# Performance work log

Measured on AMD Instinct MI355X. Metric: run time of the kernel, lower is better.

## Reference

```python
import jax, jax.numpy as jnp
import numpy as np

DEPTH = 6
N_LEAF = 2 ** DEPTH          # 64
GATE_COUNT = N_LEAF - 1      # 63
B = 1024
GATING_FEATURES = 512
IN_FEATURES = 512
OUT_FEATURES = 512


def setup_inputs() -> dict:
    key = jax.random.key(0)
    k1, k2, k3, k4 = jax.random.split(key, 4)
    x_gating = jax.random.normal(k1, (B, GATING_FEATURES), dtype=jnp.float32)
    x_leaf = jax.random.normal(k2, (B, IN_FEATURES), dtype=jnp.float32)
    # kaiming-normal-ish init scales
    gw = jax.random.normal(k3, (GATING_FEATURES, GATE_COUNT), dtype=jnp.float32) * (1.0 / np.sqrt(GATING_FEATURES))
    gb = jnp.zeros((GATE_COUNT,), dtype=jnp.float32)
    pw = jax.random.normal(k4, (OUT_FEATURES, IN_FEATURES, N_LEAF), dtype=jnp.float32) * (1.0 / np.sqrt(IN_FEATURES))
    pb = jnp.zeros((OUT_FEATURES, N_LEAF), dtype=jnp.float32)
    return {"x_gating": x_gating, "x_leaf": x_leaf, "gw": gw, "gb": gb, "pw": pw, "pb": pb}


def _leaf_probs(x_gating, gw, gb):
    # gatings: (B, gate_count), internal nodes in breadth-first order
    gatings = jax.nn.sigmoid(x_gating @ gw + gb)
    b = gatings.shape[0]
    dens = jnp.ones((b, 1), dtype=gatings.dtype)  # root density
    start = 0
    for d in range(DEPTH):
        n_par = 2 ** d
        g = gatings[:, start:start + n_par]          # (B, n_par)
        # left child (even it+1) gets g, right child gets 1-g, interleaved
        dens = jnp.stack([dens * g, dens * (1.0 - g)], axis=-1).reshape(b, 2 * n_par)
        start += n_par
    return dens  # (B, n_leaf) = leaf densities (last n_leaf node densities)


def reference(x_gating, x_leaf, gw, gb, pw, pb):
    leaf_probs = _leaf_probs(x_gating, gw, gb)              # (B, L)
    # gated projection applied to x_leaf, summed over leaves:
    # equals ((pw @ leaf_probs.T).permute(2,0,1) @ x_leaf[...,None])[...,0]
    result = jnp.einsum('oil,bl,bi->bo', pw, leaf_probs, x_leaf)
    result = result + leaf_probs @ pb.T                     # gated bias (B, O)
    return result
```

## Files before the change

### kernel.cpp

```cpp
#include <hip/hip_runtime.h>
#include <stdint.h>

#define B_SZ   1024
#define GF     512
#define GC     63
#define NLEAF  64
#define IN_F   512
#define OUT_F  512

typedef float f32x4 __attribute__((ext_vector_type(4)));
typedef __fp16 h16x2 __attribute__((ext_vector_type(2)));
typedef __fp16 h16x8 __attribute__((ext_vector_type(8)));
typedef _Float16 f16x2 __attribute__((ext_vector_type(2)));

union HF8 { f16x2 h2[4]; h16x8 v; uint4 u; };

__device__ inline f16x2 pkrtz(float a, float b) {
  union { h16x2 r; f16x2 f; } u;
  u.r = __builtin_amdgcn_cvt_pkrtz(a, b);
  return u.f;
}

__global__ __launch_bounds__(512, 2) void k_leafprobs(
    const float* __restrict__ xg, const float* __restrict__ gw,
    const float* __restrict__ gb, float* __restrict__ p_ws)
{
  __shared__ float xsr[GF];
  __shared__ float part[512];
  __shared__ float gates[GC + 1];
  const int b = blockIdx.x;
  const int t = threadIdx.x;

  xsr[t] = xg[(size_t)b * GF + t];
  __syncthreads();

  const int ks = t >> 6, g = t & 63;
  float acc = 0.f;
  if (g < GC) {
    const float* gp = gw + (size_t)(ks * 64) * GC + g;
    const float* xp = &xsr[ks * 64];
#pragma unroll 8
    for (int k = 0; k < 64; ++k) acc += xp[k] * gp[(size_t)k * GC];
  }
  part[t] = acc;
  __syncthreads();

  if (t < GC) {
    float s = gb[t];
#pragma unroll
    for (int r = 0; r < 8; ++r) s += part[r * 64 + t];
    gates[t] = 1.f / (1.f + expf(-s));
  }
  __syncthreads();

  if (t < NLEAF) {
    float v = 1.f;
    int idx = 0, start = 0;
#pragma unroll
    for (int d = 0; d < 6; ++d) {
      int bit = (t >> (5 - d)) & 1;
      float gg = gates[start + idx];
      v *= bit ? (1.f - gg) : gg;
      idx = 2 * idx + bit;
      start += (1 << d);
    }
    p_ws[(size_t)b * NLEAF + t] = v;
  }
}

#define SK 16
#define KI 32

template <bool ATOMIC>
__global__ __launch_bounds__(256, 2) void k_fused(
    const float* __restrict__ x_leaf,
    const float* __restrict__ p_ws,
    const float* __restrict__ pw,
    const float* __restrict__ pb,
    float* __restrict__ dst)
{
  __shared__ __align__(16) float         xs[KI][256];
  __shared__ __align__(16) unsigned char bs8[2 * 16384];

  const int tid  = threadIdx.x;
  const int lane = tid & 63;
  const int wid  = tid >> 6;
  const int quad = lane >> 4;
  const int l15  = lane & 15;
  const int l7   = l15 & 7;

  const int bid = blockIdx.x;
  const int nt  = bid & 7;
  const int mt  = (bid >> 3) & 3;
  const int kc  = bid >> 5;

  const int row_m0 = mt * 256;
  const int o0     = nt * 64;
  const int i0     = kc * KI;
  const int wm     = wid * 64;

  {
    const float* src = x_leaf + (size_t)(row_m0 + tid) * IN_F + i0;
#pragma unroll
    for (int q = 0; q < 8; ++q) {
      float4 v = *(const float4*)(src + q * 4);
      xs[q * 4 + 0][tid] = v.x;
      xs[q * 4 + 1][tid] = v.y;
      xs[q * 4 + 2][tid] = v.z;
      xs[q * 4 + 3][tid] = v.w;
    }
  }

  HF8 prh[4][2];
#pragma unroll
  for (int mi = 0; mi < 4; ++mi) {
    const int row = row_m0 + wm + mi * 16 + l15;
#pragma unroll
    for (int ks = 0; ks < 2; ++ks) {
      const f32x4* src = (const f32x4*)(p_ws + (size_t)row * NLEAF + ks * 32 + quad * 8);
      f32x4 lo = src[0], hi = src[1];
      prh[mi][ks].h2[0] = pkrtz(lo[0], lo[1]);
      prh[mi][ks].h2[1] = pkrtz(lo[2], lo[3]);
      prh[mi][ks].h2[2] = pkrtz(hi[0], hi[1]);
      prh[mi][ks].h2[3] = pkrtz(hi[2], hi[3]);
    }
  }

  const int br  = tid >> 2;
  const int seg = tid & 3;
  const float* bsrc0 = pw + ((size_t)(o0 + br) * IN_F + i0) * NLEAF + seg * 16;

  const int wsw   = (br & 7) << 4;
  const int woff0 = br * 128 + ((seg * 32) ^ wsw);
  const int woff1 = br * 128 + ((seg * 32 + 16) ^ wsw);
  int coff[2];
#pragma unroll
  for (int ks = 0; ks < 2; ++ks)
    coff[ks] = (ks * 64 + quad * 16) ^ (l7 << 4);
  const int rbase = l15 * 128;

  f32x4 acc[4][4];
#pragma unroll
  for (int mi = 0; mi < 4; ++mi)
#pragma unroll
    for (int ni = 0; ni < 4; ++ni)
      acc[mi][ni] = (f32x4)(0.f);

  f32x4 rb[4][4];
  HF8 afA[2][4], afB[2][4];

#define BLOAD(T, SLOT)                                                        \
  {                                                                           \
    const float* a_ = bsrc0 + (size_t)(T) * NLEAF;                            \
    asm volatile(                                                             \
        "global_load_dwordx4 %0, %4, off\n\t"                                 \
        "global_load_dwordx4 %1, %4, off offset:16\n\t"                       \
        "global_load_dwordx4 %2, %4, off offset:32\n\t"                       \
        "global_load_dwordx4 %3, %4, off offset:48"                           \
        : "=&v"(rb[SLOT][0]), "=&v"(rb[SLOT][1]),                             \
          "=&v"(rb[SLOT][2]), "=&v"(rb[SLOT][3])                              \
        : "v"(a_) : "memory");                                                \
  }

#define BWAIT_(SLOT, N)                                                       \
  asm volatile("s_waitcnt vmcnt(" #N ")"                                      \
               : "+v"(rb[SLOT][0]), "+v"(rb[SLOT][1]),                        \
                 "+v"(rb[SLOT][2]), "+v"(rb[SLOT][3])::"memory");
#define BWAIT(SLOT, N) BWAIT_(SLOT, N)

#define BSTAGE(SLOT, BUF, SUB)                                                \
  {                                                                           \
    HF8 c0_, c1_;                                                             \
    f32x4 a0_ = rb[SLOT][0], a1_ = rb[SLOT][1];                               \
    f32x4 a2_ = rb[SLOT][2], a3_ = rb[SLOT][3];                               \
    c0_.h2[0] = pkrtz(a0_[0], a0_[1]);                                        \
    c0_.h2[1] = pkrtz(a0_[2], a0_[3]);                                        \
    c0_.h2[2] = pkrtz(a1_[0], a1_[1]);                                        \
    c0_.h2[3] = pkrtz(a1_[2], a1_[3]);                                        \
    c1_.h2[0] = pkrtz(a2_[0], a2_[1]);                                        \
    c1_.h2[1] = pkrtz(a2_[2], a2_[3]);                                        \
    c1_.h2[2] = pkrtz(a3_[0], a3_[1]);                                        \
    c1_.h2[3] = pkrtz(a3_[2], a3_[3]);                                        \
    unsigned char* d_ = bs8 + (BUF) * 16384 + (SUB) * 8192;                   \
    *(uint4*)(d_ + woff0) = c0_.u;                                            \
    *(uint4*)(d_ + woff1) = c1_.u;                                            \
  }

#define BARRIER() asm volatile("s_waitcnt lgkmcnt(0)\n\ts_barrier" ::: "memory")

#define PREP(IT, AF)                                                          \
  {                                                                           \
    float xvf[4];                                                             \
    _Float16 xh[4];                                                           \
    _Pragma("unroll")                                                         \
    for (int mi = 0; mi < 4; ++mi) xvf[mi] = xs[(IT)][wm + mi * 16 + l15];    \
    _Pragma("unroll")                                                         \
    for (int mi = 0; mi < 4; ++mi) xh[mi] = (_Float16)xvf[mi];                \
    _Pragma("unroll")                                                         \
    for (int ks = 0; ks < 2; ++ks) {                                          \
      _Pragma("unroll")                                                       \
      for (int mi = 0; mi < 4; ++mi) {                                        \
        f16x2 xp_; xp_[0] = xh[mi]; xp_[1] = xh[mi];                          \
        _Pragma("unroll")                                                     \
        for (int j = 0; j < 4; ++j) AF[ks][mi].h2[j] = prh[mi][ks].h2[j] * xp_; \
      }                                                                       \
    }                                                                         \
  }

#define MFMAC(AF, BUF, SUB)                                                   \
  {                                                                           \
    const unsigned char* bsr_ = bs8 + (BUF) * 16384 + (SUB) * 8192;           \
    __builtin_amdgcn_s_setprio(1);                                            \
    _Pragma("unroll")                                                         \
    for (int ks = 0; ks < 2; ++ks) {                                          \
      _Pragma("unroll")                                                       \
      for (int ni = 0; ni < 4; ++ni) {                                        \
        h16x8 bfr = *(const h16x8*)(bsr_ + ni * 2048 + rbase + coff[ks]);     \
        _Pragma("unroll")                                                     \
        for (int mi = 0; mi < 4; ++mi)                                        \
          acc[mi][ni] = __builtin_amdgcn_mfma_f32_16x16x32_f16(               \
              AF[ks][mi].v, bfr, acc[mi][ni], 0, 0, 0);                       \
      }                                                                       \
    }                                                                         \
    __builtin_amdgcn_s_setprio(0);                                            \
  }

#define PHASE(IT0, BUF, SA, SB, WA, WB, DLA, DLB, PN)                         \
  {                                                                           \
    PREP((IT0) + 1, afB)                                                      \
    MFMAC(afA, BUF, 0)                                                        \
    BWAIT(SA, WA)                                                             \
    BSTAGE(SA, (BUF) ^ 1, 0)                                                  \
    if (DLA) { BLOAD((IT0) + 6, SA) }                                         \
    if (PN)  { PREP((IT0) + 2, afA) }                                         \
    MFMAC(afB, BUF, 1)                                                        \
    BWAIT(SB, WB)                                                             \
    BSTAGE(SB, (BUF) ^ 1, 1)                                                  \
    if (DLB) { BLOAD((IT0) + 7, SB) }                                         \
    BARRIER();                                                                \
  }

  BLOAD(0, 0)
  BLOAD(1, 1)
  BLOAD(2, 2)
  BLOAD(3, 3)
  BWAIT(0, 12)
  BSTAGE(0, 0, 0)
  BWAIT(1, 8)
  BSTAGE(1, 0, 1)
  BLOAD(4, 0)
  BLOAD(5, 1)
  BARRIER();
  PREP(0, afA)

  for (int pp = 0; pp < 24; pp += 8) {
    PHASE(pp + 0, 0, 2, 3, 12, 12, 1, 1, 1)
    PHASE(pp + 2, 1, 0, 1, 12, 12, 1, 1, 1)
    PHASE(pp + 4, 0, 2, 3, 12, 12, 1, 1, 1)
    PHASE(pp + 6, 1, 0, 1, 12, 12, 1, 1, 1)
  }
  PHASE(24, 0, 2, 3, 12, 12, 1, 1, 1)
  PHASE(26, 1, 0, 1, 12, 8, 0, 0, 1)
  PHASE(28, 0, 2, 3, 4, 0, 0, 0, 1)
  PREP(31, afB)
  MFMAC(afA, 1, 0)
  MFMAC(afB, 1, 1)

#undef BLOAD
#undef BWAIT
#undef BWAIT_
#undef BSTAGE
#undef BARRIER
#undef PREP
#undef MFMAC
#undef PHASE

  if (kc == 0) {
    {
      const float* pbs = pb + (size_t)(o0 + br) * NLEAF + seg * 16;
      float4 a0_ = *(const float4*)(pbs);
      float4 a1_ = *(const float4*)(pbs + 4);
      float4 a2_ = *(const float4*)(pbs + 8);
      float4 a3_ = *(const float4*)(pbs + 12);
      HF8 c0_, c1_;
      c0_.h2[0] = pkrtz(a0_.x, a0_.y);
      c0_.h2[1] = pkrtz(a0_.z, a0_.w);
      c0_.h2[2] = pkrtz(a1_.x, a1_.y);
      c0_.h2[3] = pkrtz(a1_.z, a1_.w);
      c1_.h2[0] = pkrtz(a2_.x, a2_.y);
      c1_.h2[1] = pkrtz(a2_.z, a2_.w);
      c1_.h2[2] = pkrtz(a3_.x, a3_.y);
      c1_.h2[3] = pkrtz(a3_.z, a3_.w);
      *(uint4*)(bs8 + woff0) = c0_.u;
      *(uint4*)(bs8 + woff1) = c1_.u;
    }
    __syncthreads();
    const unsigned char* bsr_ = bs8;
#pragma unroll
    for (int ks = 0; ks < 2; ++ks) {
#pragma unroll
      for (int ni = 0; ni < 4; ++ni) {
        h16x8 bfr = *(const h16x8*)(bsr_ + ni * 2048 + rbase + coff[ks]);
#pragma unroll
        for (int mi = 0; mi < 4; ++mi)
          acc[mi][ni] = __builtin_amdgcn_mfma_f32_16x16x32_f16(
              prh[mi][ks].v, bfr, acc[mi][ni], 0, 0, 0);
      }
    }
  }

#pragma unroll
  for (int mi = 0; mi < 4; ++mi) {
#pragma unroll
    for (int ni = 0; ni < 4; ++ni) {
      int row = row_m0 + wm + mi * 16 + quad * 4;
      int col = o0 + ni * 16 + l15;
      if (ATOMIC) {
        float* o = dst + (size_t)row * OUT_F + col;
        atomicAdd(o,             acc[mi][ni][0]);
        atomicAdd(o + OUT_F,     acc[mi][ni][1]);
        atomicAdd(o + 2 * OUT_F, acc[mi][ni][2]);
        atomicAdd(o + 3 * OUT_F, acc[mi][ni][3]);
      } else {
        float* o = dst + ((size_t)kc << 19) + (size_t)row * OUT_F + col;
        o[0]         = acc[mi][ni][0];
        o[OUT_F]     = acc[mi][ni][1];
        o[2 * OUT_F] = acc[mi][ni][2];
        o[3 * OUT_F] = acc[mi][ni][3];
      }
    }
  }
}

__global__ __launch_bounds__(256, 8) void k_reduce(
    const float* __restrict__ parts, float* __restrict__ out, int nparts)
{
  const int idx = blockIdx.x * 256 + threadIdx.x;
  f32x4 a = (f32x4)(0.f);
#pragma unroll 8
  for (int k = 0; k < nparts; ++k)
    a += ((const f32x4*)(parts + ((size_t)k << 19)))[idx];
  ((f32x4*)out)[idx] = a;
}

extern "C" void kernel_launch(void* const* d_in, const int* in_sizes, int n_in,
                              void* d_out, int out_size, void* d_ws, size_t ws_size,
                              hipStream_t stream) {
  const float* xg = (const float*)d_in[0];
  const float* xl = (const float*)d_in[1];
  const float* gw = (const float*)d_in[2];
  const float* gb = (const float*)d_in[3];
  const float* pw = (const float*)d_in[4];
  const float* pb = (const float*)d_in[5];
  float* out = (float*)d_out;

  const size_t P_BYTES = (size_t)B_SZ * NLEAF * 4;
  const size_t SLICE   = (size_t)B_SZ * OUT_F * 4;

  float* p_ws  = (float*)d_ws;
  float* parts = (float*)((char*)d_ws + P_BYTES);

  k_leafprobs<<<dim3(B_SZ), dim3(512), 0, stream>>>(xg, gw, gb, p_ws);

  if (ws_size >= P_BYTES + SK * SLICE) {
    k_fused<false><<<dim3(512), dim3(256), 0, stream>>>(xl, p_ws, pw, pb, parts);
    k_reduce<<<dim3(512), dim3(256), 0, stream>>>(parts, out, SK);
  } else {
    k_reduce<<<dim3(512), dim3(256), 0, stream>>>(parts, out, 0);
    k_fused<true><<<dim3(512), dim3(256), 0, stream>>>(xl, p_ws, pw, pb, out);
  }
}
```

Baseline: 146.4 us.

## Split fused GEMM block across 8 waves with 2-way N partition per wave

Doubles the fused kernel's block size to 512 threads, splitting each wave's output tile in half along N so each wave holds 4x2 accumulators instead of 4x4. The B-tile loads are spread over more threads with fewer in-flight slots, and the separate A-fragment prep/MFMA software pipeline is merged into a single COMPUTE step. The aim is to cut per-thread register pressure and raise wave-level parallelism to hide memory latency. In exchange, each wave recomputes the scaled A fragments redundantly, and the prefetch pipeline becomes shallower.

```diff
diff --git a/kernel.cpp b/kernel.cpp
--- a/kernel.cpp
+++ b/kernel.cpp
@@ -72,7 +72,7 @@
 #define KI 32
 
 template <bool ATOMIC>
-__global__ __launch_bounds__(256, 2) void k_fused(
+__global__ __launch_bounds__(512, 4) void k_fused(
     const float* __restrict__ x_leaf,
     const float* __restrict__ p_ws,
     const float* __restrict__ pw,
@@ -85,6 +85,8 @@
   const int tid  = threadIdx.x;
   const int lane = tid & 63;
   const int wid  = tid >> 6;
+  const int wmg  = wid >> 1;
+  const int wn   = wid & 1;
   const int quad = lane >> 4;
   const int l15  = lane & 15;
   const int l7   = l15 & 7;
@@ -97,17 +99,18 @@
   const int row_m0 = mt * 256;
   const int o0     = nt * 64;
   const int i0     = kc * KI;
-  const int wm     = wid * 64;
+  const int wm     = wmg * 64;
 
   {
-    const float* src = x_leaf + (size_t)(row_m0 + tid) * IN_F + i0;
-#pragma unroll
-    for (int q = 0; q < 8; ++q) {
+    const int r = tid & 255;
+    const int h = tid >> 8;
+    const float* src = x_leaf + (size_t)(row_m0 + r) * IN_F + i0 + h * 16;
+#pragma unroll
+    for (int q = 0; q < 4; ++q) {
       float4 v = *(const float4*)(src + q * 4);
-      xs[q * 4 + 0][tid] = v.x;
-      xs[q * 4 + 1][tid] = v.y;
-      xs[q * 4 + 2][tid] = v.z;
-      xs[q * 4 + 3][tid] = v.w;
+      const int c = h * 16 + q * 4;
+      xs[c + 0][r] = v.x; xs[c + 1][r] = v.y;
+      xs[c + 2][r] = v.z; xs[c + 3][r] = v.w;
     }
   }
 
@@ -126,69 +129,55 @@
     }
   }
 
-  const int br  = tid >> 2;
-  const int seg = tid & 3;
-  const float* bsrc0 = pw + ((size_t)(o0 + br) * IN_F + i0) * NLEAF + seg * 16;
-
-  const int wsw   = (br & 7) << 4;
-  const int woff0 = br * 128 + ((seg * 32) ^ wsw);
-  const int woff1 = br * 128 + ((seg * 32 + 16) ^ wsw);
+  const int br  = tid >> 3;
+  const int seg = tid & 7;
+  const float* bsrc0 = pw + ((size_t)(o0 + br) * IN_F + i0) * NLEAF + seg * 8;
+
+  const int woff = br * 128 + ((seg * 16) ^ ((br & 7) << 4));
   int coff[2];
 #pragma unroll
   for (int ks = 0; ks < 2; ++ks)
     coff[ks] = (ks * 64 + quad * 16) ^ (l7 << 4);
-  const int rbase = l15 * 128;
-
-  f32x4 acc[4][4];
+  const int rbase = (wn * 32 + l15) * 128;
+
+  f32x4 acc[4][2];
 #pragma unroll
   for (int mi = 0; mi < 4; ++mi)
 #pragma unroll
-    for (int ni = 0; ni < 4; ++ni)
+    for (int ni = 0; ni < 2; ++ni)
       acc[mi][ni] = (f32x4)(0.f);
 
-  f32x4 rb[4][4];
-  HF8 afA[2][4], afB[2][4];
+  f32x4 rb[2][2];
 
 #define BLOAD(T, SLOT)                                                        \
   {                                                                           \
     const float* a_ = bsrc0 + (size_t)(T) * NLEAF;                            \
     asm volatile(                                                             \
-        "global_load_dwordx4 %0, %4, off\n\t"                                 \
-        "global_load_dwordx4 %1, %4, off offset:16\n\t"                       \
-        "global_load_dwordx4 %2, %4, off offset:32\n\t"                       \
-        "global_load_dwordx4 %3, %4, off offset:48"                           \
-        : "=&v"(rb[SLOT][0]), "=&v"(rb[SLOT][1]),                             \
-          "=&v"(rb[SLOT][2]), "=&v"(rb[SLOT][3])                              \
+        "global_load_dwordx4 %0, %2, off\n\t"                                 \
+        "global_load_dwordx4 %1, %2, off offset:16"                           \
+        : "=&v"(rb[SLOT][0]), "=&v"(rb[SLOT][1])                              \
         : "v"(a_) : "memory");                                                \
   }
 
 #define BWAIT_(SLOT, N)                                                       \
   asm volatile("s_waitcnt vmcnt(" #N ")"                                      \
-               : "+v"(rb[SLOT][0]), "+v"(rb[SLOT][1]),                        \
-                 "+v"(rb[SLOT][2]), "+v"(rb[SLOT][3])::"memory");
+               : "+v"(rb[SLOT][0]), "+v"(rb[SLOT][1])::"memory");
 #define BWAIT(SLOT, N) BWAIT_(SLOT, N)
 
 #define BSTAGE(SLOT, BUF, SUB)                                                \
   {                                                                           \
-    HF8 c0_, c1_;                                                             \
+    HF8 c0_;                                                                  \
     f32x4 a0_ = rb[SLOT][0], a1_ = rb[SLOT][1];                               \
-    f32x4 a2_ = rb[SLOT][2], a3_ = rb[SLOT][3];                               \
     c0_.h2[0] = pkrtz(a0_[0], a0_[1]);                                        \
     c0_.h2[1] = pkrtz(a0_[2], a0_[3]);                                        \
     c0_.h2[2] = pkrtz(a1_[0], a1_[1]);                                        \
     c0_.h2[3] = pkrtz(a1_[2], a1_[3]);                                        \
-    c1_.h2[0] = pkrtz(a2_[0], a2_[1]);                                        \
-    c1_.h2[1] = pkrtz(a2_[2], a2_[3]);                                        \
-    c1_.h2[2] = pkrtz(a3_[0], a3_[1]);                                        \
-    c1_.h2[3] = pkrtz(a3_[2], a3_[3]);                                        \
-    unsigned char* d_ = bs8 + (BUF) * 16384 + (SUB) * 8192;                   \
-    *(uint4*)(d_ + woff0) = c0_.u;                                            \
-    *(uint4*)(d_ + woff1) = c1_.u;                                            \
+    *(uint4*)(bs8 + (BUF) * 16384 + (SUB) * 8192 + woff) = c0_.u;             \
   }
 
 #define BARRIER() asm volatile("s_waitcnt lgkmcnt(0)\n\ts_barrier" ::: "memory")
 
-#define PREP(IT, AF)                                                          \
+#define COMPUTE(IT, BUF, SUB)                                                 \
   {                                                                           \
     float xvf[4];                                                             \
     _Float16 xh[4];                                                           \
@@ -196,110 +185,88 @@
     for (int mi = 0; mi < 4; ++mi) xvf[mi] = xs[(IT)][wm + mi * 16 + l15];    \
     _Pragma("unroll")                                                         \
     for (int mi = 0; mi < 4; ++mi) xh[mi] = (_Float16)xvf[mi];                \
-    _Pragma("unroll")                                                         \
-    for (int ks = 0; ks < 2; ++ks) {                                          \
-      _Pragma("unroll")                                                       \
-      for (int mi = 0; mi < 4; ++mi) {                                        \
-        f16x2 xp_; xp_[0] = xh[mi]; xp_[1] = xh[mi];                          \
-        _Pragma("unroll")                                                     \
-        for (int j = 0; j < 4; ++j) AF[ks][mi].h2[j] = prh[mi][ks].h2[j] * xp_; \
-      }                                                                       \
-    }                                                                         \
-  }
-
-#define MFMAC(AF, BUF, SUB)                                                   \
-  {                                                                           \
     const unsigned char* bsr_ = bs8 + (BUF) * 16384 + (SUB) * 8192;           \
     __builtin_amdgcn_s_setprio(1);                                            \
     _Pragma("unroll")                                                         \
     for (int ks = 0; ks < 2; ++ks) {                                          \
+      h16x8 af[4];                                                            \
       _Pragma("unroll")                                                       \
-      for (int ni = 0; ni < 4; ++ni) {                                        \
+      for (int mi = 0; mi < 4; ++mi) {                                        \
+        HF8 t_;                                                               \
+        f16x2 xp_; xp_[0] = xh[mi]; xp_[1] = xh[mi];                          \
+        _Pragma("unroll")                                                     \
+        for (int j = 0; j < 4; ++j) t_.h2[j] = prh[mi][ks].h2[j] * xp_;       \
+        af[mi] = t_.v;                                                        \
+      }                                                                       \
+      _Pragma("unroll")                                                       \
+      for (int ni = 0; ni < 2; ++ni) {                                        \
         h16x8 bfr = *(const h16x8*)(bsr_ + ni * 2048 + rbase + coff[ks]);     \
         _Pragma("unroll")                                                     \
         for (int mi = 0; mi < 4; ++mi)                                        \
           acc[mi][ni] = __builtin_amdgcn_mfma_f32_16x16x32_f16(               \
-              AF[ks][mi].v, bfr, acc[mi][ni], 0, 0, 0);                       \
+              af[mi], bfr, acc[mi][ni], 0, 0, 0);                             \
       }                                                                       \
     }                                                                         \
     __builtin_amdgcn_s_setprio(0);                                            \
   }
 
-#define PHASE(IT0, BUF, SA, SB, WA, WB, DLA, DLB, PN)                         \
+#define PHASE(IT0, BUF, WA, WB, DL)                                           \
   {                                                                           \
-    PREP((IT0) + 1, afB)                                                      \
-    MFMAC(afA, BUF, 0)                                                        \
-    BWAIT(SA, WA)                                                             \
-    BSTAGE(SA, (BUF) ^ 1, 0)                                                  \
-    if (DLA) { BLOAD((IT0) + 6, SA) }                                         \
-    if (PN)  { PREP((IT0) + 2, afA) }                                         \
-    MFMAC(afB, BUF, 1)                                                        \
-    BWAIT(SB, WB)                                                             \
-    BSTAGE(SB, (BUF) ^ 1, 1)                                                  \
-    if (DLB) { BLOAD((IT0) + 7, SB) }                                         \
+    COMPUTE(IT0, BUF, 0)                                                      \
+    BWAIT(0, WA)                                                              \
+    BSTAGE(0, (BUF) ^ 1, 0)                                                   \
+    if (DL) { BLOAD((IT0) + 4, 0) }                                           \
+    COMPUTE((IT0) + 1, BUF, 1)                                                \
+    BWAIT(1, WB)                                                              \
+    BSTAGE(1, (BUF) ^ 1, 1)                                                   \
+    if (DL) { BLOAD((IT0) + 5, 1) }                                           \
     BARRIER();                                                                \
   }
 
   BLOAD(0, 0)
   BLOAD(1, 1)
-  BLOAD(2, 2)
-  BLOAD(3, 3)
-  BWAIT(0, 12)
+  BWAIT(0, 2)
   BSTAGE(0, 0, 0)
-  BWAIT(1, 8)
+  BLOAD(2, 0)
+  BWAIT(1, 2)
   BSTAGE(1, 0, 1)
-  BLOAD(4, 0)
-  BLOAD(5, 1)
+  BLOAD(3, 1)
   BARRIER();
-  PREP(0, afA)
-
-  for (int pp = 0; pp < 24; pp += 8) {
-    PHASE(pp + 0, 0, 2, 3, 12, 12, 1, 1, 1)
-    PHASE(pp + 2, 1, 0, 1, 12, 12, 1, 1, 1)
-    PHASE(pp + 4, 0, 2, 3, 12, 12, 1, 1, 1)
-    PHASE(pp + 6, 1, 0, 1, 12, 12, 1, 1, 1)
-  }
-  PHASE(24, 0, 2, 3, 12, 12, 1, 1, 1)
-  PHASE(26, 1, 0, 1, 12, 8, 0, 0, 1)
-  PHASE(28, 0, 2, 3, 4, 0, 0, 0, 1)
-  PREP(31, afB)
-  MFMAC(afA, 1, 0)
-  MFMAC(afB, 1, 1)
+
+  for (int it0 = 0; it0 < 28; it0 += 4) {
+    PHASE(it0 + 0, 0, 2, 2, 1)
+    PHASE(it0 + 2, 1, 2, 2, 1)
+  }
+  PHASE(28, 0, 2, 0, 0)
+  COMPUTE(30, 1, 0)
+  COMPUTE(31, 1, 1)
 
 #undef BLOAD
 #undef BWAIT
 #undef BWAIT_
 #undef BSTAGE
 #undef BARRIER
-#undef PREP
-#undef MFMAC
+#undef COMPUTE
 #undef PHASE
 
   if (kc == 0) {
     {
-      const float* pbs = pb + (size_t)(o0 + br) * NLEAF + seg * 16;
+      const float* pbs = pb + (size_t)(o0 + br) * NLEAF + seg * 8;
       float4 a0_ = *(const float4*)(pbs);
       float4 a1_ = *(const float4*)(pbs + 4);
-      float4 a2_ = *(const float4*)(pbs + 8);
-      float4 a3_ = *(const float4*)(pbs + 12);
-      HF8 c0_, c1_;
+      HF8 c0_;
       c0_.h2[0] = pkrtz(a0_.x, a0_.y);
       c0_.h2[1] = pkrtz(a0_.z, a0_.w);
       c0_.h2[2] = pkrtz(a1_.x, a1_.y);
       c0_.h2[3] = pkrtz(a1_.z, a1_.w);
-      c1_.h2[0] = pkrtz(a2_.x, a2_.y);
-      c1_.h2[1] = pkrtz(a2_.z, a2_.w);
-      c1_.h2[2] = pkrtz(a3_.x, a3_.y);
-      c1_.h2[3] = pkrtz(a3_.z, a3_.w);
-      *(uint4*)(bs8 + woff0) = c0_.u;
-      *(uint4*)(bs8 + woff1) = c1_.u;
+      *(uint4*)(bs8 + woff) = c0_.u;
     }
     __syncthreads();
     const unsigned char* bsr_ = bs8;
 #pragma unroll
     for (int ks = 0; ks < 2; ++ks) {
 #pragma unroll
-      for (int ni = 0; ni < 4; ++ni) {
+      for (int ni = 0; ni < 2; ++ni) {
         h16x8 bfr = *(const h16x8*)(bsr_ + ni * 2048 + rbase + coff[ks]);
 #pragma unroll
         for (int mi = 0; mi < 4; ++mi)
@@ -312,9 +279,9 @@
 #pragma unroll
   for (int mi = 0; mi < 4; ++mi) {
 #pragma unroll
-    for (int ni = 0; ni < 4; ++ni) {
+    for (int ni = 0; ni < 2; ++ni) {
       int row = row_m0 + wm + mi * 16 + quad * 4;
-      int col = o0 + ni * 16 + l15;
+      int col = o0 + wn * 32 + ni * 16 + l15;
       if (ATOMIC) {
         float* o = dst + (size_t)row * OUT_F + col;
         atomicAdd(o,             acc[mi][ni][0]);
@@ -363,10 +330,10 @@
   k_leafprobs<<<dim3(B_SZ), dim3(512), 0, stream>>>(xg, gw, gb, p_ws);
 
   if (ws_size >= P_BYTES + SK * SLICE) {
-    k_fused<false><<<dim3(512), dim3(256), 0, stream>>>(xl, p_ws, pw, pb, parts);
+    k_fused<false><<<dim3(512), dim3(512), 0, stream>>>(xl, p_ws, pw, pb, parts);
     k_reduce<<<dim3(512), dim3(256), 0, stream>>>(parts, out, SK);
   } else {
     k_reduce<<<dim3(512), dim3(256), 0, stream>>>(parts, out, 0);
-    k_fused<true><<<dim3(512), dim3(256), 0, stream>>>(xl, p_ws, pw, pb, out);
-  }
-}
+    k_fused<true><<<dim3(512), dim3(512), 0, stream>>>(xl, p_ws, pw, pb, out);
+  }
+}
```

New measurement: 149.3 us. 2.0% more time.

## Deepen pw prefetch pipeline to six register slots and three LDS sub-stages

Applied to the files above, without the earlier changes.

Restructures the main K-loop so that each barrier phase processes three iterations instead of two. Each LDS buffer now holds three sub-tiles, and six register slots keep global loads of pw in flight, so more load latency is hidden and fewer barriers are issued. The separate A-fragment prefetch (PREP/MFMAC split with setprio) is merged into an inline COMPUTE step. x_leaf is also stored in LDS as fp16 to halve its footprint. In exchange, register pressure and LDS use go up, which risks lower occupancy, and the explicit A-fragment/MFMA overlap is lost.

```diff
diff --git a/kernel.cpp b/kernel.cpp
--- a/kernel.cpp
+++ b/kernel.cpp
@@ -12,8 +12,10 @@
 typedef __fp16 h16x2 __attribute__((ext_vector_type(2)));
 typedef __fp16 h16x8 __attribute__((ext_vector_type(8)));
 typedef _Float16 f16x2 __attribute__((ext_vector_type(2)));
+typedef unsigned short ushort;
 
 union HF8 { f16x2 h2[4]; h16x8 v; uint4 u; };
+union HU  { ushort u; _Float16 f; };
 
 __device__ inline f16x2 pkrtz(float a, float b) {
   union { h16x2 r; f16x2 f; } u;
@@ -79,8 +81,8 @@
     const float* __restrict__ pb,
     float* __restrict__ dst)
 {
-  __shared__ __align__(16) float         xs[KI][256];
-  __shared__ __align__(16) unsigned char bs8[2 * 16384];
+  __shared__ __align__(16) ushort        xs_h[KI][256];
+  __shared__ __align__(16) unsigned char bs8[2 * 24576];
 
   const int tid  = threadIdx.x;
   const int lane = tid & 63;
@@ -104,10 +106,13 @@
 #pragma unroll
     for (int q = 0; q < 8; ++q) {
       float4 v = *(const float4*)(src + q * 4);
-      xs[q * 4 + 0][tid] = v.x;
-      xs[q * 4 + 1][tid] = v.y;
-      xs[q * 4 + 2][tid] = v.z;
-      xs[q * 4 + 3][tid] = v.w;
+      HU t0, t1, t2, t3;
+      t0.f = (_Float16)v.x; t1.f = (_Float16)v.y;
+      t2.f = (_Float16)v.z; t3.f = (_Float16)v.w;
+      xs_h[q * 4 + 0][tid] = t0.u;
+      xs_h[q * 4 + 1][tid] = t1.u;
+      xs_h[q * 4 + 2][tid] = t2.u;
+      xs_h[q * 4 + 3][tid] = t3.u;
     }
   }
 
@@ -146,8 +151,7 @@
     for (int ni = 0; ni < 4; ++ni)
       acc[mi][ni] = (f32x4)(0.f);
 
-  f32x4 rb[4][4];
-  HF8 afA[2][4], afB[2][4];
+  f32x4 rb[6][4];
 
 #define BLOAD(T, SLOT)                                                        \
   {                                                                           \
@@ -181,62 +185,57 @@
     c1_.h2[1] = pkrtz(a2_[2], a2_[3]);                                        \
     c1_.h2[2] = pkrtz(a3_[0], a3_[1]);                                        \
     c1_.h2[3] = pkrtz(a3_[2], a3_[3]);                                        \
-    unsigned char* d_ = bs8 + (BUF) * 16384 + (SUB) * 8192;                   \
+    unsigned char* d_ = bs8 + (BUF) * 24576 + (SUB) * 8192;                   \
     *(uint4*)(d_ + woff0) = c0_.u;                                            \
     *(uint4*)(d_ + woff1) = c1_.u;                                            \
   }
 
 #define BARRIER() asm volatile("s_waitcnt lgkmcnt(0)\n\ts_barrier" ::: "memory")
 
-#define PREP(IT, AF)                                                          \
+#define COMPUTE(IT, BUF, SUB)                                                 \
   {                                                                           \
-    float xvf[4];                                                             \
     _Float16 xh[4];                                                           \
     _Pragma("unroll")                                                         \
-    for (int mi = 0; mi < 4; ++mi) xvf[mi] = xs[(IT)][wm + mi * 16 + l15];    \
-    _Pragma("unroll")                                                         \
-    for (int mi = 0; mi < 4; ++mi) xh[mi] = (_Float16)xvf[mi];                \
+    for (int mi = 0; mi < 4; ++mi) {                                          \
+      HU t_; t_.u = xs_h[(IT)][wm + mi * 16 + l15]; xh[mi] = t_.f;            \
+    }                                                                         \
+    const unsigned char* bsr_ = bs8 + (BUF) * 24576 + (SUB) * 8192;           \
     _Pragma("unroll")                                                         \
     for (int ks = 0; ks < 2; ++ks) {                                          \
+      h16x8 af[4];                                                            \
       _Pragma("unroll")                                                       \
       for (int mi = 0; mi < 4; ++mi) {                                        \
+        HF8 t_;                                                               \
         f16x2 xp_; xp_[0] = xh[mi]; xp_[1] = xh[mi];                          \
         _Pragma("unroll")                                                     \
-        for (int j = 0; j < 4; ++j) AF[ks][mi].h2[j] = prh[mi][ks].h2[j] * xp_; \
+        for (int j = 0; j < 4; ++j) t_.h2[j] = prh[mi][ks].h2[j] * xp_;       \
+        af[mi] = t_.v;                                                        \
       }                                                                       \
-    }                                                                         \
-  }
-
-#define MFMAC(AF, BUF, SUB)                                                   \
-  {                                                                           \
-    const unsigned char* bsr_ = bs8 + (BUF) * 16384 + (SUB) * 8192;           \
-    __builtin_amdgcn_s_setprio(1);                                            \
-    _Pragma("unroll")                                                         \
-    for (int ks = 0; ks < 2; ++ks) {                                          \
       _Pragma("unroll")                                                       \
       for (int ni = 0; ni < 4; ++ni) {                                        \
         h16x8 bfr = *(const h16x8*)(bsr_ + ni * 2048 + rbase + coff[ks]);     \
         _Pragma("unroll")                                                     \
         for (int mi = 0; mi < 4; ++mi)                                        \
           acc[mi][ni] = __builtin_amdgcn_mfma_f32_16x16x32_f16(               \
-              AF[ks][mi].v, bfr, acc[mi][ni], 0, 0, 0);                       \
+              af[mi], bfr, acc[mi][ni], 0, 0, 0);                             \
       }                                                                       \
     }                                                                         \
-    __builtin_amdgcn_s_setprio(0);                                            \
-  }
-
-#define PHASE(IT0, BUF, SA, SB, WA, WB, DLA, DLB, PN)                         \
+  }
+
+#define PHASE(IT0, BUF, SB, W1, W2, W3, D1, D2, D3)                           \
   {                                                                           \
-    PREP((IT0) + 1, afB)                                                      \
-    MFMAC(afA, BUF, 0)                                                        \
-    BWAIT(SA, WA)                                                             \
-    BSTAGE(SA, (BUF) ^ 1, 0)                                                  \
-    if (DLA) { BLOAD((IT0) + 6, SA) }                                         \
-    if (PN)  { PREP((IT0) + 2, afA) }                                         \
-    MFMAC(afB, BUF, 1)                                                        \
-    BWAIT(SB, WB)                                                             \
-    BSTAGE(SB, (BUF) ^ 1, 1)                                                  \
-    if (DLB) { BLOAD((IT0) + 7, SB) }                                         \
+    COMPUTE(IT0, BUF, 0)                                                      \
+    BWAIT(SB, W1)                                                             \
+    BSTAGE(SB, (BUF) ^ 1, 0)                                                  \
+    if (D1) { BLOAD((IT0) + 9, SB) }                                          \
+    COMPUTE((IT0) + 1, BUF, 1)                                                \
+    BWAIT((SB) + 1, W2)                                                       \
+    BSTAGE((SB) + 1, (BUF) ^ 1, 1)                                            \
+    if (D2) { BLOAD((IT0) + 10, (SB) + 1) }                                   \
+    COMPUTE((IT0) + 2, BUF, 2)                                                \
+    BWAIT((SB) + 2, W3)                                                       \
+    BSTAGE((SB) + 2, (BUF) ^ 1, 2)                                            \
+    if (D3) { BLOAD((IT0) + 11, (SB) + 2) }                                   \
     BARRIER();                                                                \
   }
 
@@ -244,35 +243,45 @@
   BLOAD(1, 1)
   BLOAD(2, 2)
   BLOAD(3, 3)
-  BWAIT(0, 12)
+  BLOAD(4, 4)
+  BLOAD(5, 5)
+  BWAIT(0, 20)
   BSTAGE(0, 0, 0)
-  BWAIT(1, 8)
+  BLOAD(6, 0)
+  BWAIT(1, 20)
   BSTAGE(1, 0, 1)
-  BLOAD(4, 0)
-  BLOAD(5, 1)
+  BLOAD(7, 1)
+  BWAIT(2, 20)
+  BSTAGE(2, 0, 2)
+  BLOAD(8, 2)
   BARRIER();
-  PREP(0, afA)
-
-  for (int pp = 0; pp < 24; pp += 8) {
-    PHASE(pp + 0, 0, 2, 3, 12, 12, 1, 1, 1)
-    PHASE(pp + 2, 1, 0, 1, 12, 12, 1, 1, 1)
-    PHASE(pp + 4, 0, 2, 3, 12, 12, 1, 1, 1)
-    PHASE(pp + 6, 1, 0, 1, 12, 12, 1, 1, 1)
-  }
-  PHASE(24, 0, 2, 3, 12, 12, 1, 1, 1)
-  PHASE(26, 1, 0, 1, 12, 8, 0, 0, 1)
-  PHASE(28, 0, 2, 3, 4, 0, 0, 0, 1)
-  PREP(31, afB)
-  MFMAC(afA, 1, 0)
-  MFMAC(afB, 1, 1)
+
+  PHASE(0,  0, 3, 20, 20, 20, 1, 1, 1)
+  PHASE(3,  1, 0, 20, 20, 20, 1, 1, 1)
+  PHASE(6,  0, 3, 20, 20, 20, 1, 1, 1)
+  PHASE(9,  1, 0, 20, 20, 20, 1, 1, 1)
+  PHASE(12, 0, 3, 20, 20, 20, 1, 1, 1)
+  PHASE(15, 1, 0, 20, 20, 20, 1, 1, 1)
+  PHASE(18, 0, 3, 20, 20, 20, 1, 1, 1)
+  PHASE(21, 1, 0, 20, 20, 20, 1, 1, 0)
+  PHASE(24, 0, 3, 16, 12, 8, 0, 0, 0)
+  COMPUTE(27, 1, 0)
+  BWAIT(0, 4)
+  BSTAGE(0, 0, 0)
+  COMPUTE(28, 1, 1)
+  BWAIT(1, 0)
+  BSTAGE(1, 0, 1)
+  COMPUTE(29, 1, 2)
+  BARRIER();
+  COMPUTE(30, 0, 0)
+  COMPUTE(31, 0, 1)
 
 #undef BLOAD
 #undef BWAIT
 #undef BWAIT_
 #undef BSTAGE
 #undef BARRIER
-#undef PREP
-#undef MFMAC
+#undef COMPUTE
 #undef PHASE
 
   if (kc == 0) {
@@ -291,11 +300,11 @@
       c1_.h2[1] = pkrtz(a2_.z, a2_.w);
       c1_.h2[2] = pkrtz(a3_.x, a3_.y);
       c1_.h2[3] = pkrtz(a3_.z, a3_.w);
-      *(uint4*)(bs8 + woff0) = c0_.u;
-      *(uint4*)(bs8 + woff1) = c1_.u;
+      *(uint4*)(bs8 + 24576 + woff0) = c0_.u;
+      *(uint4*)(bs8 + 24576 + woff1) = c1_.u;
     }
     __syncthreads();
-    const unsigned char* bsr_ = bs8;
+    const unsigned char* bsr_ = bs8 + 24576;
 #pragma unroll
     for (int ks = 0; ks < 2; ++ks) {
 #pragma unroll
```

Result: slower. 150.2 us (+2.6%).
